# Performance work log

Measured on AMD Instinct MI355X. Metric: run time of the kernel, lower is better.

The kernel has to match this reference:

```python
import jax, jax.numpy as jnp
import numpy as np

B, S, H = 1, 2048, 2880
NH, HD = 64, 64            # num_attention_heads, head_dim
NKV = 8                    # num_key_value_heads
GROUPS = NH // NKV         # 8
RANK = 384                 # kv_lora_rank
ROPE_BASE = 150000.0
NEG = -3.4e38              # additive mask value (finfo min-ish)


def setup_inputs() -> dict:
    key = jax.random.key(0)
    ks = jax.random.split(key, 8)
    init = 0.02
    hidden_states = jax.random.normal(ks[0], (B, S, H), dtype=jnp.float32)
    # causal additive mask [B,1,S,S]
    causal = jnp.tril(jnp.ones((S, S), dtype=bool))
    attention_mask = jnp.where(causal, 0.0, NEG).astype(jnp.float32)[None, None]
    attention_mask = jnp.broadcast_to(attention_mask, (B, 1, S, S))
    q_w = jax.random.normal(ks[1], (NH * HD, H), dtype=jnp.float32) * init
    q_b = jnp.zeros((NH * HD,), dtype=jnp.float32)
    kv_a_w = jax.random.normal(ks[2], (RANK, H), dtype=jnp.float32) * init
    kv_b_w = jax.random.normal(ks[3], (NKV * HD * 2, RANK), dtype=jnp.float32) * init
    o_w = jax.random.normal(ks[4], (H, NH * HD), dtype=jnp.float32) * init
    o_b = jnp.zeros((H,), dtype=jnp.float32)
    return {"hidden_states": hidden_states, "attention_mask": attention_mask,
            "q_w": q_w, "q_b": q_b, "kv_a_w": kv_a_w, "kv_b_w": kv_b_w,
            "o_w": o_w, "o_b": o_b}


def _rotate_half(x):
    x1, x2 = x[..., : x.shape[-1] // 2], x[..., x.shape[-1] // 2:]
    return jnp.concatenate((-x2, x1), axis=-1)


def _rope_cos_sin(S, dtype):
    inv_freq = 1.0 / (ROPE_BASE ** (jnp.arange(0, HD, 2, dtype=jnp.float32) / HD))
    pos = jnp.arange(S, dtype=jnp.float32)
    freqs = pos[:, None] * inv_freq[None, :]          # [S, HD/2]
    emb = jnp.concatenate((freqs, freqs), axis=-1)    # [S, HD]
    # [1, 1, S, HD] to broadcast over batch and heads
    return jnp.cos(emb).astype(dtype)[None, None], jnp.sin(emb).astype(dtype)[None, None]


def reference(hidden_states, attention_mask, q_w, q_b, kv_a_w, kv_b_w, o_w, o_b):
    B, S, H = hidden_states.shape
    # Q projection -> [B, NH, S, HD]
    q = (hidden_states @ q_w.T + q_b).reshape(B, S, NH, HD).transpose(0, 2, 1, 3)
    # compressed KV -> decompress
    compressed_kv = hidden_states @ kv_a_w.T                 # [B, S, RANK]
    kv = (compressed_kv @ kv_b_w.T).reshape(B, S, NKV, 2 * HD)
    k, v = kv[..., :HD], kv[..., HD:]
    k = k.transpose(0, 2, 1, 3)                              # [B, NKV, S, HD]
    v = v.transpose(0, 2, 1, 3)
    # full-dim RoPE (module applies rotary over entire head_dim)
    cos, sin = _rope_cos_sin(S, q.dtype)
    q = q * cos + _rotate_half(q) * sin
    k = k * cos + _rotate_half(k) * sin
    # GQA expand: repeat_interleave over head axis
    k = jnp.repeat(k, GROUPS, axis=1)                        # [B, NH, S, HD]
    v = jnp.repeat(v, GROUPS, axis=1)
    scores = jnp.einsum('bhqd,bhkd->bhqk', q, k) / np.sqrt(HD)
    scores = scores + attention_mask
    probs = jax.nn.softmax(scores.astype(jnp.float32), axis=-1).astype(q.dtype)
    attn = jnp.einsum('bhqk,bhkd->bhqd', probs, v)           # [B, NH, S, HD]
    attn = attn.transpose(0, 2, 1, 3).reshape(B, S, NH * HD)
    return attn @ o_w.T + o_b
```

## Files before the change

### kernel.cpp

```cpp
#include <hip/hip_runtime.h>
#include <math.h>

typedef unsigned short u16;
typedef unsigned int u32;
typedef float f4 __attribute__((ext_vector_type(4)));
typedef short bf16x8 __attribute__((ext_vector_type(8)));
typedef float f32x4 __attribute__((ext_vector_type(4)));

#define S_LEN 2048
#define H_DIM 2880
#define NQD 4096
#define RANKD 384
#define HD 64
#define NH 64
#define NKV 8
#define RLN 0.37244970541f

__device__ __forceinline__ u16 f2bf(float f) {
  u32 u = __float_as_uint(f);
  u += 0x7fffu + ((u >> 16) & 1u);
  return (u16)(u >> 16);
}

#define GLOAD_LDS(g, l) __builtin_amdgcn_global_load_lds( \
    (__attribute__((address_space(1))) void*)(g),          \
    (__attribute__((address_space(3))) void*)(l), 16, 0, 0)

__device__ __forceinline__ size_t koff_s(int s) {
  return (size_t)((s >> 6) * 4096 + ((s >> 4) & 3) * 1024 + (s & 15) * 8);
}
__device__ __forceinline__ int koff_d(int d) {
  return (d >> 5) * 512 + ((d >> 3) & 3) * 128 + (d & 7);
}
__device__ __forceinline__ size_t voff_s(int s) {
  return (size_t)((s >> 6) * 4096 + ((s >> 5) & 1) * 512 + ((s >> 3) & 3) * 128 + (s & 7));
}
__device__ __forceinline__ int voff_d(int d) {
  return ((d >> 4) & 3) * 1024 + (d & 15) * 8;
}

__global__ void conv_f2b(const float* __restrict__ in, u16* __restrict__ out, int n4) {
  int i = blockIdx.x * blockDim.x + threadIdx.x;
  if (i >= n4) return;
  f4 v = ((const f4*)in)[i];
  ushort4 o;
  o.x = f2bf(v[0]); o.y = f2bf(v[1]); o.z = f2bf(v[2]); o.w = f2bf(v[3]);
  ((ushort4*)out)[i] = o;
}

__global__ __launch_bounds__(256) void gemm128(
    const u16* __restrict__ A, const u16* __restrict__ W,
    const float* __restrict__ bias, int K,
    u16* __restrict__ out0) {
  __shared__ __align__(16) u16 As[128 * 32];
  __shared__ __align__(16) u16 Bs[128 * 32];
  int t = threadIdx.x, w = t >> 6, L = t & 63;
  int lm = L & 15, quad = L >> 4;
  int m0 = blockIdx.x * 128, n0 = blockIdx.y * 128;
  int wm = w >> 1, wn = w & 1;
  int srow = L >> 2, scol8 = (L & 3) * 8;
  const u16* Ag0 = A + (size_t)(m0 + (w * 2) * 16 + srow) * K + scol8;
  const u16* Ag1 = Ag0 + (size_t)16 * K;
  const u16* Wg0 = W + (size_t)(n0 + (w * 2) * 16 + srow) * K + scol8;
  const u16* Wg1 = Wg0 + (size_t)16 * K;
  u16* lA0 = &As[(w * 2) * 512];
  u16* lA1 = &As[(w * 2 + 1) * 512];
  u16* lB0 = &Bs[(w * 2) * 512];
  u16* lB1 = &Bs[(w * 2 + 1) * 512];
  f32x4 acc[4][4] = {};
  int nk = K >> 5;
  for (int kt = 0; kt < nk; ++kt) {
    GLOAD_LDS(Ag0, lA0);
    GLOAD_LDS(Ag1, lA1);
    GLOAD_LDS(Wg0, lB0);
    GLOAD_LDS(Wg1, lB1);
    Ag0 += 32; Ag1 += 32; Wg0 += 32; Wg1 += 32;
    __syncthreads();
    bf16x8 af[4], bf[4];
#pragma unroll
    for (int i = 0; i < 4; ++i) af[i] = *(const bf16x8*)&As[(wm * 64 + i * 16 + lm) * 32 + quad * 8];
#pragma unroll
    for (int j = 0; j < 4; ++j) bf[j] = *(const bf16x8*)&Bs[(wn * 64 + j * 16 + lm) * 32 + quad * 8];
#pragma unroll
    for (int i = 0; i < 4; ++i)
#pragma unroll
      for (int j = 0; j < 4; ++j)
        acc[i][j] = __builtin_amdgcn_mfma_f32_16x16x32_bf16(af[i], bf[j], acc[i][j], 0, 0, 0);
    __syncthreads();
  }
  int head = (n0 + wn * 64) >> 6;
  float b0v = bias[head * 64 + lm];
  float b1v = bias[head * 64 + 16 + lm];
  float b2v = bias[head * 64 + 32 + lm];
  float b3v = bias[head * 64 + 48 + lm];
  float invf1 = __expf(-(float)lm * RLN);
  float invf2 = __expf(-(float)(lm + 16) * RLN);
#pragma unroll
  for (int i = 0; i < 4; ++i) {
    int sq = m0 + wm * 64 + i * 16 + quad * 4;
#pragma unroll
    for (int r = 0; r < 4; ++r) {
      float a0 = acc[i][0][r] + b0v, a1 = acc[i][1][r] + b1v;
      float a2 = acc[i][2][r] + b2v, a3 = acc[i][3][r] + b3v;
      float s1, c1, s2, c2;
      sincosf((float)(sq + r) * invf1, &s1, &c1);
      sincosf((float)(sq + r) * invf2, &s2, &c2);
      u16* op = out0 + ((size_t)head * S_LEN + sq + r) * HD;
      op[lm]      = f2bf((a0 * c1 - a2 * s1) * 0.125f);
      op[lm + 32] = f2bf((a2 * c1 + a0 * s1) * 0.125f);
      op[lm + 16] = f2bf((a1 * c2 - a3 * s2) * 0.125f);
      op[lm + 48] = f2bf((a3 * c2 + a1 * s2) * 0.125f);
    }
  }
}

__global__ __launch_bounds__(256) void gemm64(
    const u16* __restrict__ A, const u16* __restrict__ W,
    const float* __restrict__ bias, int K, int Nreal,
    float* __restrict__ out) {
  __shared__ __align__(16) u16 As[64 * 32];
  __shared__ __align__(16) u16 Bs[128 * 32];
  int t = threadIdx.x, w = t >> 6, L = t & 63;
  int lm = L & 15, quad = L >> 4;
  int m0 = blockIdx.x * 64, n0 = blockIdx.y * 128;
  int wm = w >> 1, wn = w & 1;
  int srow = L >> 2, scol8 = (L & 3) * 8;
  const u16* Ag = A + (size_t)(m0 + w * 16 + srow) * K + scol8;
  int wr0 = n0 + w * 16 + srow;      if (wr0 > Nreal - 1) wr0 = Nreal - 1;
  int wr1 = n0 + 64 + w * 16 + srow; if (wr1 > Nreal - 1) wr1 = Nreal - 1;
  const u16* Wg0 = W + (size_t)wr0 * K + scol8;
  const u16* Wg1 = W + (size_t)wr1 * K + scol8;
  u16* lA  = &As[w * 512];
  u16* lB0 = &Bs[w * 512];
  u16* lB1 = &Bs[2048 + w * 512];
  f32x4 acc[2][4] = {};
  int nk = K >> 5;
  for (int kt = 0; kt < nk; ++kt) {
    GLOAD_LDS(Ag, lA);
    GLOAD_LDS(Wg0, lB0);
    GLOAD_LDS(Wg1, lB1);
    Ag += 32; Wg0 += 32; Wg1 += 32;
    __syncthreads();
    bf16x8 af[2], bf[4];
#pragma unroll
    for (int i = 0; i < 2; ++i) af[i] = *(const bf16x8*)&As[(wm * 32 + i * 16 + lm) * 32 + quad * 8];
#pragma unroll
    for (int j = 0; j < 4; ++j) bf[j] = *(const bf16x8*)&Bs[(wn * 64 + j * 16 + lm) * 32 + quad * 8];
#pragma unroll
    for (int i = 0; i < 2; ++i)
#pragma unroll
      for (int j = 0; j < 4; ++j)
        acc[i][j] = __builtin_amdgcn_mfma_f32_16x16x32_bf16(af[i], bf[j], acc[i][j], 0, 0, 0);
    __syncthreads();
  }
#pragma unroll
  for (int i = 0; i < 2; ++i) {
#pragma unroll
    for (int r = 0; r < 4; ++r) {
      int row = m0 + wm * 32 + i * 16 + quad * 4 + r;
#pragma unroll
      for (int j = 0; j < 4; ++j) {
        int col = n0 + wn * 64 + j * 16 + lm;
        if (col < Nreal)
          out[(size_t)row * Nreal + col] = acc[i][j][r] + bias[col];
      }
    }
  }
}

__global__ __launch_bounds__(256) void gemm_bt(
    const u16* __restrict__ A, const u16* __restrict__ W,
    int M, int N, int K, int mode,
    u16* __restrict__ out0, u16* __restrict__ out1) {
  __shared__ __align__(16) u16 As[64 * 32];
  __shared__ __align__(16) u16 Bs[64 * 32];
  int t = threadIdx.x;
  int m0 = blockIdx.x * 64, n0 = blockIdx.y * 64;
  int w = t >> 6, L = t & 63;
  int srow = t >> 2, scol = (t & 3) * 8;
  int lm = L & 15, quad = L >> 4;
  const u16* Ap = A + (size_t)(m0 + srow) * K + scol;
  const u16* Wp = W + (size_t)(n0 + srow) * K + scol;
  f32x4 acc0 = {0.f, 0.f, 0.f, 0.f}, acc1 = acc0, acc2 = acc0, acc3 = acc0;
  int aoff = (w * 16 + lm) * 32 + quad * 8;
  int boff = lm * 32 + quad * 8;
  int nk = K >> 5;
  uint4 av = *(const uint4*)Ap;
  uint4 wv = *(const uint4*)Wp;
  for (int kt = 0; kt < nk; ++kt) {
    *(uint4*)&As[srow * 32 + scol] = av;
    *(uint4*)&Bs[srow * 32 + scol] = wv;
    __syncthreads();
    if (kt + 1 < nk) {
      Ap += 32; Wp += 32;
      av = *(const uint4*)Ap;
      wv = *(const uint4*)Wp;
    }
    bf16x8 af = *(const bf16x8*)&As[aoff];
    bf16x8 b0 = *(const bf16x8*)&Bs[boff];
    bf16x8 b1 = *(const bf16x8*)&Bs[boff + 16 * 32];
    bf16x8 b2 = *(const bf16x8*)&Bs[boff + 32 * 32];
    bf16x8 b3 = *(const bf16x8*)&Bs[boff + 48 * 32];
    acc0 = __builtin_amdgcn_mfma_f32_16x16x32_bf16(af, b0, acc0, 0, 0, 0);
    acc1 = __builtin_amdgcn_mfma_f32_16x16x32_bf16(af, b1, acc1, 0, 0, 0);
    acc2 = __builtin_amdgcn_mfma_f32_16x16x32_bf16(af, b2, acc2, 0, 0, 0);
    acc3 = __builtin_amdgcn_mfma_f32_16x16x32_bf16(af, b3, acc3, 0, 0, 0);
    __syncthreads();
  }
  int mbase = m0 + w * 16 + quad * 4;
  if (mode == 3) {
    for (int r = 0; r < 4; ++r) {
      int row = mbase + r;
      float vals[4] = {acc0[r], acc1[r], acc2[r], acc3[r]};
      for (int nt = 0; nt < 4; ++nt)
        out0[(size_t)row * N + (n0 + nt * 16 + lm)] = f2bf(vals[nt]);
    }
  } else {
    bool isV = ((blockIdx.y & 1) == 1);
    int head = (n0 >> 7);
    size_t hb = (size_t)head << 17;
    if (isV) {
      int dof[4];
#pragma unroll
      for (int nt = 0; nt < 4; ++nt) dof[nt] = voff_d(nt * 16 + lm);
      for (int r = 0; r < 4; ++r) {
        int s = mbase + r;
        size_t so = hb + voff_s(s);
        float vals[4] = {acc0[r], acc1[r], acc2[r], acc3[r]};
#pragma unroll
        for (int nt = 0; nt < 4; ++nt)
          out1[so + dof[nt]] = f2bf(vals[nt]);
      }
    } else {
      int d0 = koff_d(lm), d1 = koff_d(lm + 16), d2 = koff_d(lm + 32), d3 = koff_d(lm + 48);
      float invf1 = __expf(-(float)lm * RLN);
      float invf2 = __expf(-(float)(lm + 16) * RLN);
      for (int r = 0; r < 4; ++r) {
        int s = mbase + r;
        float a0 = acc0[r], a1 = acc1[r], a2 = acc2[r], a3 = acc3[r];
        float s1, c1, s2, c2;
        sincosf((float)s * invf1, &s1, &c1);
        sincosf((float)s * invf2, &s2, &c2);
        size_t so = hb + koff_s(s);
        out0[so + d0] = f2bf(a0 * c1 - a2 * s1);
        out0[so + d2] = f2bf(a2 * c1 + a0 * s1);
        out0[so + d1] = f2bf(a1 * c2 - a3 * s2);
        out0[so + d3] = f2bf(a3 * c2 + a1 * s2);
      }
    }
  }
}

__global__ __launch_bounds__(256, 4) void attn_v3(
    const u16* __restrict__ Qb, const u16* __restrict__ Kf,
    const u16* __restrict__ Vf, u16* __restrict__ attnb) {
  __shared__ __align__(16) u16 Ps[4 * 16 * 72];
  int t = threadIdx.x;
  int w = t >> 6, L = t & 63;
  int lm = L & 15, quad = L >> 4;
  int bx = blockIdx.x, h = blockIdx.y, kvh = h >> 3;
  u16* pw = &Ps[w * 16 * 72];
  const u16* Kbase = Kf + ((size_t)kvh << 17) + L * 8;
  const u16* Vbase = Vf + ((size_t)kvh << 17) + L * 8;

  for (int ph = 0; ph < 2; ++ph) {
    int qt = ph ? (31 - bx) : bx;
    int q0 = qt * 64;
    const u16* Qp = Qb + ((size_t)h * S_LEN + q0 + w * 16 + lm) * HD + quad * 8;
    bf16x8 qf0 = *(const bf16x8*)Qp;
    bf16x8 qf1 = *(const bf16x8*)(Qp + 32);
    f32x4 o[4] = {};
    float m_ = -3.0e38f, l_ = 0.f;

    for (int c = 0; c <= qt; ++c) {
      const u16* Kc = Kbase + (size_t)c * 4096;
      bf16x8 kfa[4], kfb[4];
#pragma unroll
      for (int j = 0; j < 4; ++j) {
        kfa[j] = *(const bf16x8*)(Kc + j * 1024);
        kfb[j] = *(const bf16x8*)(Kc + j * 1024 + 512);
      }
      f32x4 st[4] = {};
#pragma unroll
      for (int j = 0; j < 4; ++j) {
        st[j] = __builtin_amdgcn_mfma_f32_16x16x32_bf16(kfa[j], qf0, st[j], 0, 0, 0);
        st[j] = __builtin_amdgcn_mfma_f32_16x16x32_bf16(kfb[j], qf1, st[j], 0, 0, 0);
      }
      const u16* Vc = Vbase + (size_t)c * 4096;
      bf16x8 vfa[4], vfb[4];
#pragma unroll
      for (int j = 0; j < 4; ++j) {
        vfa[j] = *(const bf16x8*)(Vc + j * 1024);
        vfb[j] = *(const bf16x8*)(Vc + j * 1024 + 512);
      }
      if (c == qt) {
        int qloc = w * 16 + lm;
#pragma unroll
        for (int j = 0; j < 4; ++j) {
          int kvb = j * 16 + quad * 4;
#pragma unroll
          for (int r = 0; r < 4; ++r)
            if (kvb + r > qloc) st[j][r] = -3.0e38f;
        }
      }
      float mloc = -3.0e38f;
#pragma unroll
      for (int j = 0; j < 4; ++j)
        mloc = fmaxf(mloc, fmaxf(fmaxf(st[j][0], st[j][1]), fmaxf(st[j][2], st[j][3])));
      mloc = fmaxf(mloc, __shfl_xor(mloc, 16));
      mloc = fmaxf(mloc, __shfl_xor(mloc, 32));
      float mn = fmaxf(m_, mloc);
      float al = __expf(m_ - mn);
      m_ = mn;
      float sum = 0.f;
      u16* pws = pw + lm * 72;
#pragma unroll
      for (int j = 0; j < 4; ++j) {
        float p0 = __expf(st[j][0] - mn);
        float p1 = __expf(st[j][1] - mn);
        float p2 = __expf(st[j][2] - mn);
        float p3 = __expf(st[j][3] - mn);
        sum += (p0 + p1) + (p2 + p3);
        uint2 pk;
        pk.x = (u32)f2bf(p0) | ((u32)f2bf(p1) << 16);
        pk.y = (u32)f2bf(p2) | ((u32)f2bf(p3) << 16);
        *(uint2*)(pws + j * 16 + quad * 4) = pk;
      }
      l_ = l_ * al + sum;
      float a0 = __shfl(al, quad * 4 + 0);
      float a1 = __shfl(al, quad * 4 + 1);
      float a2 = __shfl(al, quad * 4 + 2);
      float a3 = __shfl(al, quad * 4 + 3);
#pragma unroll
      for (int j = 0; j < 4; ++j) {
        o[j][0] *= a0; o[j][1] *= a1; o[j][2] *= a2; o[j][3] *= a3;
      }
      bf16x8 pa = *(const bf16x8*)(pw + lm * 72 + quad * 8);
      bf16x8 pb = *(const bf16x8*)(pw + lm * 72 + 32 + quad * 8);
#pragma unroll
      for (int j = 0; j < 4; ++j) {
        o[j] = __builtin_amdgcn_mfma_f32_16x16x32_bf16(pa, vfa[j], o[j], 0, 0, 0);
        o[j] = __builtin_amdgcn_mfma_f32_16x16x32_bf16(pb, vfb[j], o[j], 0, 0, 0);
      }
    }
    l_ += __shfl_xor(l_, 16);
    l_ += __shfl_xor(l_, 32);
    float linv = 1.0f / l_;
    float li0 = __shfl(linv, quad * 4 + 0);
    float li1 = __shfl(linv, quad * 4 + 1);
    float li2 = __shfl(linv, quad * 4 + 2);
    float li3 = __shfl(linv, quad * 4 + 3);
#pragma unroll
    for (int r = 0; r < 4; ++r) {
      float lr = (r == 0) ? li0 : (r == 1) ? li1 : (r == 2) ? li2 : li3;
      int row = q0 + w * 16 + quad * 4 + r;
      u16* op = attnb + (size_t)row * NQD + h * HD;
      op[lm]      = f2bf(o[0][r] * lr);
      op[lm + 16] = f2bf(o[1][r] * lr);
      op[lm + 32] = f2bf(o[2][r] * lr);
      op[lm + 48] = f2bf(o[3][r] * lr);
    }
  }
}

extern "C" void kernel_launch(void* const* d_in, const int* in_sizes, int n_in,
                              void* d_out, int out_size, void* d_ws, size_t ws_size,
                              hipStream_t stream) {
  (void)in_sizes; (void)n_in; (void)out_size; (void)ws_size;
  const float* hidden = (const float*)d_in[0];
  const float* q_w    = (const float*)d_in[2];
  const float* q_b    = (const float*)d_in[3];
  const float* kv_a_w = (const float*)d_in[4];
  const float* kv_b_w = (const float*)d_in[5];
  const float* o_w    = (const float*)d_in[6];
  const float* o_b    = (const float*)d_in[7];

  char* ws = (char*)d_ws;
  u16* hb    = (u16*)(ws + 0);
  u16* qwb   = (u16*)(ws + 11796480);
  u16* kab   = (u16*)(ws + 35389440);
  u16* kbb   = (u16*)(ws + 37601280);
  u16* owb   = (u16*)(ws + 38387712);
  u16* Qb    = (u16*)(ws + 61980672);
  u16* CKVb  = (u16*)(ws + 78757888);
  u16* Kfb   = (u16*)(ws + 80330752);
  u16* Vfb   = (u16*)(ws + 82427904);
  u16* attnb = (u16*)(ws + 84525056);

  conv_f2b<<<(1474560 + 255) / 256, 256, 0, stream>>>(hidden, hb, 1474560);
  conv_f2b<<<(2949120 + 255) / 256, 256, 0, stream>>>(q_w, qwb, 2949120);
  conv_f2b<<<(276480 + 255) / 256, 256, 0, stream>>>(kv_a_w, kab, 276480);
  conv_f2b<<<(98304 + 255) / 256, 256, 0, stream>>>(kv_b_w, kbb, 98304);
  conv_f2b<<<(2949120 + 255) / 256, 256, 0, stream>>>(o_w, owb, 2949120);

  gemm128<<<dim3(16, 32), 256, 0, stream>>>(hb, qwb, q_b, H_DIM, Qb);
  gemm_bt<<<dim3(32, 6),  256, 0, stream>>>(hb, kab, S_LEN, RANKD, H_DIM, 3, CKVb, nullptr);
  gemm_bt<<<dim3(32, 16), 256, 0, stream>>>(CKVb, kbb, S_LEN, 1024, RANKD, 2, Kfb, Vfb);
  attn_v3<<<dim3(16, 64), 256, 0, stream>>>(Qb, Kfb, Vfb, attnb);
  gemm64<<<dim3(32, 23), 256, 0, stream>>>(attnb, owb, o_b, NQD, H_DIM, (float*)d_out);
}
```

Baseline: 455.5 us.

## Double-buffer LDS tiles in projection GEMMs to overlap loads with MFMA

Both GEMM kernels now keep two LDS buffers per operand, prefetching the next K-tile with global_load_lds while MFMAs run on the current tile. This aims to hide global-memory latency that previously stalled each iteration before compute. It doubles LDS use per block, which could lower occupancy. The end-of-loop sync is assumed to guard the buffer being refilled.

```diff
diff --git a/kernel.cpp b/kernel.cpp
--- a/kernel.cpp
+++ b/kernel.cpp
@@ -52,8 +52,8 @@
     const u16* __restrict__ A, const u16* __restrict__ W,
     const float* __restrict__ bias, int K,
     u16* __restrict__ out0) {
-  __shared__ __align__(16) u16 As[128 * 32];
-  __shared__ __align__(16) u16 Bs[128 * 32];
+  __shared__ __align__(16) u16 As[2 * 128 * 32];
+  __shared__ __align__(16) u16 Bs[2 * 128 * 32];
   int t = threadIdx.x, w = t >> 6, L = t & 63;
   int lm = L & 15, quad = L >> 4;
   int m0 = blockIdx.x * 128, n0 = blockIdx.y * 128;
@@ -69,18 +69,27 @@
   u16* lB1 = &Bs[(w * 2 + 1) * 512];
   f32x4 acc[4][4] = {};
   int nk = K >> 5;
+  GLOAD_LDS(Ag0, lA0);
+  GLOAD_LDS(Ag1, lA1);
+  GLOAD_LDS(Wg0, lB0);
+  GLOAD_LDS(Wg1, lB1);
+  Ag0 += 32; Ag1 += 32; Wg0 += 32; Wg1 += 32;
+  __syncthreads();
   for (int kt = 0; kt < nk; ++kt) {
-    GLOAD_LDS(Ag0, lA0);
-    GLOAD_LDS(Ag1, lA1);
-    GLOAD_LDS(Wg0, lB0);
-    GLOAD_LDS(Wg1, lB1);
-    Ag0 += 32; Ag1 += 32; Wg0 += 32; Wg1 += 32;
-    __syncthreads();
+    int cur = (kt & 1) << 12;
+    int nxt = 4096 - cur;
+    if (kt + 1 < nk) {
+      GLOAD_LDS(Ag0, lA0 + nxt);
+      GLOAD_LDS(Ag1, lA1 + nxt);
+      GLOAD_LDS(Wg0, lB0 + nxt);
+      GLOAD_LDS(Wg1, lB1 + nxt);
+      Ag0 += 32; Ag1 += 32; Wg0 += 32; Wg1 += 32;
+    }
     bf16x8 af[4], bf[4];
 #pragma unroll
-    for (int i = 0; i < 4; ++i) af[i] = *(const bf16x8*)&As[(wm * 64 + i * 16 + lm) * 32 + quad * 8];
-#pragma unroll
-    for (int j = 0; j < 4; ++j) bf[j] = *(const bf16x8*)&Bs[(wn * 64 + j * 16 + lm) * 32 + quad * 8];
+    for (int i = 0; i < 4; ++i) af[i] = *(const bf16x8*)&As[cur + (wm * 64 + i * 16 + lm) * 32 + quad * 8];
+#pragma unroll
+    for (int j = 0; j < 4; ++j) bf[j] = *(const bf16x8*)&Bs[cur + (wn * 64 + j * 16 + lm) * 32 + quad * 8];
 #pragma unroll
     for (int i = 0; i < 4; ++i)
 #pragma unroll
@@ -118,8 +127,8 @@
     const u16* __restrict__ A, const u16* __restrict__ W,
     const float* __restrict__ bias, int K, int Nreal,
     float* __restrict__ out) {
-  __shared__ __align__(16) u16 As[64 * 32];
-  __shared__ __align__(16) u16 Bs[128 * 32];
+  __shared__ __align__(16) u16 As[2 * 64 * 32];
+  __shared__ __align__(16) u16 Bs[2 * 128 * 32];
   int t = threadIdx.x, w = t >> 6, L = t & 63;
   int lm = L & 15, quad = L >> 4;
   int m0 = blockIdx.x * 64, n0 = blockIdx.y * 128;
@@ -135,17 +144,26 @@
   u16* lB1 = &Bs[2048 + w * 512];
   f32x4 acc[2][4] = {};
   int nk = K >> 5;
+  GLOAD_LDS(Ag, lA);
+  GLOAD_LDS(Wg0, lB0);
+  GLOAD_LDS(Wg1, lB1);
+  Ag += 32; Wg0 += 32; Wg1 += 32;
+  __syncthreads();
   for (int kt = 0; kt < nk; ++kt) {
-    GLOAD_LDS(Ag, lA);
-    GLOAD_LDS(Wg0, lB0);
-    GLOAD_LDS(Wg1, lB1);
-    Ag += 32; Wg0 += 32; Wg1 += 32;
-    __syncthreads();
+    int curA = (kt & 1) << 11;
+    int curB = (kt & 1) << 12;
+    int nxtA = 2048 - curA, nxtB = 4096 - curB;
+    if (kt + 1 < nk) {
+      GLOAD_LDS(Ag, lA + nxtA);
+      GLOAD_LDS(Wg0, lB0 + nxtB);
+      GLOAD_LDS(Wg1, lB1 + nxtB);
+      Ag += 32; Wg0 += 32; Wg1 += 32;
+    }
     bf16x8 af[2], bf[4];
 #pragma unroll
-    for (int i = 0; i < 2; ++i) af[i] = *(const bf16x8*)&As[(wm * 32 + i * 16 + lm) * 32 + quad * 8];
-#pragma unroll
-    for (int j = 0; j < 4; ++j) bf[j] = *(const bf16x8*)&Bs[(wn * 64 + j * 16 + lm) * 32 + quad * 8];
+    for (int i = 0; i < 2; ++i) af[i] = *(const bf16x8*)&As[curA + (wm * 32 + i * 16 + lm) * 32 + quad * 8];
+#pragma unroll
+    for (int j = 0; j < 4; ++j) bf[j] = *(const bf16x8*)&Bs[curB + (wn * 64 + j * 16 + lm) * 32 + quad * 8];
 #pragma unroll
     for (int i = 0; i < 2; ++i)
 #pragma unroll
```

Measured after the change: 443.1 us. 1.03x faster.

## Double-buffer LDS and widen K-step to 64 in projection GEMMs

Applied to the files above, without the earlier changes.

Both projection GEMM kernels now keep two LDS buffers and prefetch the next 64-wide K slab via global_load_lds while running MFMAs on the current one. Each iteration covers twice as much K, which halves the number of barriers. The aim is to hide global-memory latency behind compute and cut synchronisation overhead. In exchange each block uses four times as much LDS, which may lower occupancy, and K must be a multiple of 64 (2880 and 384 both are).

```diff
diff --git a/kernel.cpp b/kernel.cpp
--- a/kernel.cpp
+++ b/kernel.cpp
@@ -52,8 +52,8 @@
     const u16* __restrict__ A, const u16* __restrict__ W,
     const float* __restrict__ bias, int K,
     u16* __restrict__ out0) {
-  __shared__ __align__(16) u16 As[128 * 32];
-  __shared__ __align__(16) u16 Bs[128 * 32];
+  __shared__ __align__(16) u16 As[2 * 2 * 128 * 32];
+  __shared__ __align__(16) u16 Bs[2 * 2 * 128 * 32];
   int t = threadIdx.x, w = t >> 6, L = t & 63;
   int lm = L & 15, quad = L >> 4;
   int m0 = blockIdx.x * 128, n0 = blockIdx.y * 128;
@@ -68,24 +68,37 @@
   u16* lB0 = &Bs[(w * 2) * 512];
   u16* lB1 = &Bs[(w * 2 + 1) * 512];
   f32x4 acc[4][4] = {};
-  int nk = K >> 5;
+  int nk = K >> 6;
+  GLOAD_LDS(Ag0, lA0);           GLOAD_LDS(Ag1, lA1);
+  GLOAD_LDS(Ag0 + 32, lA0 + 4096); GLOAD_LDS(Ag1 + 32, lA1 + 4096);
+  GLOAD_LDS(Wg0, lB0);           GLOAD_LDS(Wg1, lB1);
+  GLOAD_LDS(Wg0 + 32, lB0 + 4096); GLOAD_LDS(Wg1 + 32, lB1 + 4096);
+  Ag0 += 64; Ag1 += 64; Wg0 += 64; Wg1 += 64;
+  __syncthreads();
   for (int kt = 0; kt < nk; ++kt) {
-    GLOAD_LDS(Ag0, lA0);
-    GLOAD_LDS(Ag1, lA1);
-    GLOAD_LDS(Wg0, lB0);
-    GLOAD_LDS(Wg1, lB1);
-    Ag0 += 32; Ag1 += 32; Wg0 += 32; Wg1 += 32;
-    __syncthreads();
-    bf16x8 af[4], bf[4];
-#pragma unroll
-    for (int i = 0; i < 4; ++i) af[i] = *(const bf16x8*)&As[(wm * 64 + i * 16 + lm) * 32 + quad * 8];
-#pragma unroll
-    for (int j = 0; j < 4; ++j) bf[j] = *(const bf16x8*)&Bs[(wn * 64 + j * 16 + lm) * 32 + quad * 8];
-#pragma unroll
-    for (int i = 0; i < 4; ++i)
-#pragma unroll
-      for (int j = 0; j < 4; ++j)
-        acc[i][j] = __builtin_amdgcn_mfma_f32_16x16x32_bf16(af[i], bf[j], acc[i][j], 0, 0, 0);
+    int cur = (kt & 1) << 13;
+    int nxt = 8192 - cur;
+    if (kt + 1 < nk) {
+      GLOAD_LDS(Ag0, lA0 + nxt);           GLOAD_LDS(Ag1, lA1 + nxt);
+      GLOAD_LDS(Ag0 + 32, lA0 + nxt + 4096); GLOAD_LDS(Ag1 + 32, lA1 + nxt + 4096);
+      GLOAD_LDS(Wg0, lB0 + nxt);           GLOAD_LDS(Wg1, lB1 + nxt);
+      GLOAD_LDS(Wg0 + 32, lB0 + nxt + 4096); GLOAD_LDS(Wg1 + 32, lB1 + nxt + 4096);
+      Ag0 += 64; Ag1 += 64; Wg0 += 64; Wg1 += 64;
+    }
+#pragma unroll
+    for (int h = 0; h < 2; ++h) {
+      int base = cur + h * 4096;
+      bf16x8 af[4], bf[4];
+#pragma unroll
+      for (int i = 0; i < 4; ++i) af[i] = *(const bf16x8*)&As[base + (wm * 64 + i * 16 + lm) * 32 + quad * 8];
+#pragma unroll
+      for (int j = 0; j < 4; ++j) bf[j] = *(const bf16x8*)&Bs[base + (wn * 64 + j * 16 + lm) * 32 + quad * 8];
+#pragma unroll
+      for (int i = 0; i < 4; ++i)
+#pragma unroll
+        for (int j = 0; j < 4; ++j)
+          acc[i][j] = __builtin_amdgcn_mfma_f32_16x16x32_bf16(af[i], bf[j], acc[i][j], 0, 0, 0);
+    }
     __syncthreads();
   }
   int head = (n0 + wn * 64) >> 6;
@@ -118,8 +131,8 @@
     const u16* __restrict__ A, const u16* __restrict__ W,
     const float* __restrict__ bias, int K, int Nreal,
     float* __restrict__ out) {
-  __shared__ __align__(16) u16 As[64 * 32];
-  __shared__ __align__(16) u16 Bs[128 * 32];
+  __shared__ __align__(16) u16 As[2 * 2 * 64 * 32];
+  __shared__ __align__(16) u16 Bs[2 * 2 * 128 * 32];
   int t = threadIdx.x, w = t >> 6, L = t & 63;
   int lm = L & 15, quad = L >> 4;
   int m0 = blockIdx.x * 64, n0 = blockIdx.y * 128;
@@ -134,23 +147,37 @@
   u16* lB0 = &Bs[w * 512];
   u16* lB1 = &Bs[2048 + w * 512];
   f32x4 acc[2][4] = {};
-  int nk = K >> 5;
+  int nk = K >> 6;
+  GLOAD_LDS(Ag, lA);            GLOAD_LDS(Ag + 32, lA + 2048);
+  GLOAD_LDS(Wg0, lB0);          GLOAD_LDS(Wg0 + 32, lB0 + 4096);
+  GLOAD_LDS(Wg1, lB1);          GLOAD_LDS(Wg1 + 32, lB1 + 4096);
+  Ag += 64; Wg0 += 64; Wg1 += 64;
+  __syncthreads();
   for (int kt = 0; kt < nk; ++kt) {
-    GLOAD_LDS(Ag, lA);
-    GLOAD_LDS(Wg0, lB0);
-    GLOAD_LDS(Wg1, lB1);
-    Ag += 32; Wg0 += 32; Wg1 += 32;
-    __syncthreads();
-    bf16x8 af[2], bf[4];
-#pragma unroll
-    for (int i = 0; i < 2; ++i) af[i] = *(const bf16x8*)&As[(wm * 32 + i * 16 + lm) * 32 + quad * 8];
-#pragma unroll
-    for (int j = 0; j < 4; ++j) bf[j] = *(const bf16x8*)&Bs[(wn * 64 + j * 16 + lm) * 32 + quad * 8];
-#pragma unroll
-    for (int i = 0; i < 2; ++i)
-#pragma unroll
-      for (int j = 0; j < 4; ++j)
-        acc[i][j] = __builtin_amdgcn_mfma_f32_16x16x32_bf16(af[i], bf[j], acc[i][j], 0, 0, 0);
+    int curA = (kt & 1) << 12;
+    int curB = (kt & 1) << 13;
+    int nxtA = 4096 - curA, nxtB = 8192 - curB;
+    if (kt + 1 < nk) {
+      GLOAD_LDS(Ag, lA + nxtA);          GLOAD_LDS(Ag + 32, lA + nxtA + 2048);
+      GLOAD_LDS(Wg0, lB0 + nxtB);        GLOAD_LDS(Wg0 + 32, lB0 + nxtB + 4096);
+      GLOAD_LDS(Wg1, lB1 + nxtB);        GLOAD_LDS(Wg1 + 32, lB1 + nxtB + 4096);
+      Ag += 64; Wg0 += 64; Wg1 += 64;
+    }
+#pragma unroll
+    for (int h = 0; h < 2; ++h) {
+      int baseA = curA + h * 2048;
+      int baseB = curB + h * 4096;
+      bf16x8 af[2], bf[4];
+#pragma unroll
+      for (int i = 0; i < 2; ++i) af[i] = *(const bf16x8*)&As[baseA + (wm * 32 + i * 16 + lm) * 32 + quad * 8];
+#pragma unroll
+      for (int j = 0; j < 4; ++j) bf[j] = *(const bf16x8*)&Bs[baseB + (wn * 64 + j * 16 + lm) * 32 + quad * 8];
+#pragma unroll
+      for (int i = 0; i < 2; ++i)
+#pragma unroll
+        for (int j = 0; j < 4; ++j)
+          acc[i][j] = __builtin_amdgcn_mfma_f32_16x16x32_bf16(af[i], bf[j], acc[i][j], 0, 0, 0);
+    }
     __syncthreads();
   }
 #pragma unroll
```

New measurement: 421.3 us. 1.08x faster.
